# Optimization experiments

Hardware: AMD Instinct MI355X
Metric: run time of the kernel (lower is better)

Reference implementation:

```python
import jax, jax.numpy as jnp
import numpy as np
from jax import lax

MAXIMIZE = True  # matches init_kwargs

def setup_inputs() -> dict:
    key = jax.random.key(0)
    cost_matrix = jax.random.normal(key, (1024, 16384), dtype=jnp.float32)
    return {"cost_matrix": cost_matrix}

def _greedy_assign(cost_matrix):
    n_rows, n_cols = cost_matrix.shape
    n_assign = min(n_rows, n_cols)
    # maximize=True -> keep costs as-is; else negate (matches torch module)
    costs = cost_matrix if MAXIMIZE else -cost_matrix
    neg_inf = jnp.array(-jnp.inf, dtype=costs.dtype)

    def step(carry, _):
        row_used, col_used = carry  # bool [n_rows], bool [n_cols]
        mask = row_used[:, None] | col_used[None, :]
        masked = jnp.where(mask, neg_inf, costs)
        flat = jnp.argmax(masked)  # row-major flat argmax, same as torch reshape(-1).argmax()
        r = flat // n_cols
        c = flat % n_cols
        row_used = row_used.at[r].set(True)
        col_used = col_used.at[c].set(True)
        return (row_used, col_used), (r, c)

    init = (jnp.zeros(n_rows, dtype=bool), jnp.zeros(n_cols, dtype=bool))
    _, (rows, cols) = lax.scan(step, init, None, length=n_assign)
    rows = rows.astype(jnp.int64) if rows.dtype != jnp.int64 else rows
    cols = cols.astype(jnp.int64) if cols.dtype != jnp.int64 else cols
    sort_idx = jnp.argsort(rows)
    return rows[sort_idx], cols[sort_idx]

def reference(cost_matrix):
    row_ind, col_ind = _greedy_assign(cost_matrix)
    return (row_ind, col_ind)
```

## Files before the change

kernel.cpp:

```cpp
#include <hip/hip_runtime.h>
#include <stdint.h>

#define NROWS 1024
#define NCOLS 16384
#define NROUNDS 3

typedef unsigned long long u64;
typedef unsigned int u32;

__device__ u64 g_rowbest[NROWS];
__device__ u64 g_colbest[NCOLS];
__device__ int g_col_used[NCOLS];
__device__ int g_row_assigned[NROWS];
__device__ int g_col_of_row[NROWS];
__device__ int g_remaining[NROWS];
__device__ int g_nrem;

__device__ __forceinline__ u32 fsort(float x) {
    u32 u = __float_as_uint(x);
    return u ^ ((u32)((int)u >> 31) | 0x80000000u);
}

__global__ void k_init(int* __restrict__ out) {
    int i = blockIdx.x * blockDim.x + threadIdx.x;
    if (i < NCOLS) { g_colbest[i] = 0ULL; g_col_used[i] = 0; }
    if (i < NROWS) {
        g_rowbest[i] = 0ULL; g_col_of_row[i] = 0; g_row_assigned[i] = 0;
        out[i] = i;
    }
    if (i == 0) g_nrem = 0;
}

__global__ void k_rowmax(const float* __restrict__ cost) {
    int r = blockIdx.x;
    const float4* row = (const float4*)(cost + (size_t)r * NCOLS);
    u64 best = 0ULL;
    for (int k = threadIdx.x; k < NCOLS / 4; k += blockDim.x) {
        float4 v = row[k];
        int c0 = k * 4;
        u64 k0 = ((u64)fsort(v.x) << 32) | (u32)(NCOLS - 1 - (c0 + 0));
        u64 k1 = ((u64)fsort(v.y) << 32) | (u32)(NCOLS - 1 - (c0 + 1));
        u64 k2 = ((u64)fsort(v.z) << 32) | (u32)(NCOLS - 1 - (c0 + 2));
        u64 k3 = ((u64)fsort(v.w) << 32) | (u32)(NCOLS - 1 - (c0 + 3));
        if (k0 > best) best = k0;
        if (k1 > best) best = k1;
        if (k2 > best) best = k2;
        if (k3 > best) best = k3;
    }
    for (int off = 32; off; off >>= 1) {
        u64 o = __shfl_down(best, off);
        if (o > best) best = o;
    }
    __shared__ u64 part[4];
    int wave = threadIdx.x >> 6;
    if ((threadIdx.x & 63) == 0) part[wave] = best;
    __syncthreads();
    if (threadIdx.x == 0) {
        u64 b = part[0];
        for (int w = 1; w < 4; w++) if (part[w] > b) b = part[w];
        g_rowbest[r] = b;
    }
}

__global__ void k_colmax(const float* __restrict__ cost) {
    int c0 = blockIdx.x * 1024 + threadIdx.x * 4;
    int r0 = blockIdx.y * 64;
    u64 b0 = 0, b1 = 0, b2 = 0, b3 = 0;
    for (int r = r0; r < r0 + 64; ++r) {
        float4 v = *(const float4*)(cost + (size_t)r * NCOLS + c0);
        u32 rk = (u32)(NROWS - 1 - r);
        u64 k0 = ((u64)fsort(v.x) << 32) | rk;
        u64 k1 = ((u64)fsort(v.y) << 32) | rk;
        u64 k2 = ((u64)fsort(v.z) << 32) | rk;
        u64 k3 = ((u64)fsort(v.w) << 32) | rk;
        if (k0 > b0) b0 = k0;
        if (k1 > b1) b1 = k1;
        if (k2 > b2) b2 = k2;
        if (k3 > b3) b3 = k3;
    }
    atomicMax(&g_colbest[c0 + 0], b0);
    atomicMax(&g_colbest[c0 + 1], b1);
    atomicMax(&g_colbest[c0 + 2], b2);
    atomicMax(&g_colbest[c0 + 3], b3);
}

__global__ void k_commit1(int* __restrict__ out) {
    int r = threadIdx.x;
    u64 key = g_rowbest[r];
    int c = NCOLS - 1 - (int)(key & 0xFFFFFFFFu);
    u64 mykey_at_c = (key & 0xFFFFFFFF00000000ULL) | (u32)(NROWS - 1 - r);
    if (g_colbest[c] == mykey_at_c) {
        g_col_used[c] = 1;
        g_col_of_row[r] = c;
        g_row_assigned[r] = 1;
        out[NROWS + r] = c;
    } else {
        int p = atomicAdd(&g_nrem, 1);
        g_remaining[p] = r;
    }
}

__global__ void k_recompute(const float* __restrict__ cost) {
    int r = blockIdx.x;
    if (g_row_assigned[r]) return;
    u64 key = g_rowbest[r];
    int cbest = NCOLS - 1 - (int)(key & 0xFFFFFFFFu);
    if (!g_col_used[cbest]) return;

    u64 best = 0ULL;
    const float4* row = (const float4*)(cost + (size_t)r * NCOLS);
    const int4* used = (const int4*)g_col_used;
    for (int k = threadIdx.x; k < NCOLS / 4; k += blockDim.x) {
        float4 v = row[k];
        int4 u = used[k];
        int c0 = k * 4;
        if (!u.x) { u64 kk = ((u64)fsort(v.x) << 32) | (u32)(NCOLS - 1 - (c0 + 0)); if (kk > best) best = kk; }
        if (!u.y) { u64 kk = ((u64)fsort(v.y) << 32) | (u32)(NCOLS - 1 - (c0 + 1)); if (kk > best) best = kk; }
        if (!u.z) { u64 kk = ((u64)fsort(v.z) << 32) | (u32)(NCOLS - 1 - (c0 + 2)); if (kk > best) best = kk; }
        if (!u.w) { u64 kk = ((u64)fsort(v.w) << 32) | (u32)(NCOLS - 1 - (c0 + 3)); if (kk > best) best = kk; }
    }
    for (int off = 32; off; off >>= 1) {
        u64 o = __shfl_down(best, off);
        if (o > best) best = o;
    }
    __shared__ u64 part[4];
    int wave = threadIdx.x >> 6;
    if ((threadIdx.x & 63) == 0) part[wave] = best;
    __syncthreads();
    if (threadIdx.x == 0) {
        u64 b = part[0];
        for (int w = 1; w < 4; w++) if (part[w] > b) b = part[w];
        g_rowbest[r] = b;
    }
}

__global__ void k_round(const float* __restrict__ cost, int* __restrict__ out) {
    __shared__ int s_list[NROWS];
    __shared__ int s_cand[NROWS];
    __shared__ u64 s_mine[NROWS];
    __shared__ u64 s_max[NROWS];
    __shared__ int s_n;
    int tid = threadIdx.x;
    if (tid == 0) s_n = 0;
    __syncthreads();
    int r = tid;
    bool unassigned = !g_row_assigned[r];
    int mypos = -1;
    if (unassigned) { mypos = atomicAdd(&s_n, 1); s_list[mypos] = r; }
    __syncthreads();
    int n = s_n;
    if (n == 0) { if (tid == 0) g_nrem = 0; return; }

    if (unassigned) {
        u64 key = g_rowbest[r];
        int c = NCOLS - 1 - (int)(key & 0xFFFFFFFFu);
        s_cand[mypos] = c;
        s_mine[mypos] = (key & 0xFFFFFFFF00000000ULL) | (u32)(NROWS - 1 - r);
        s_max[mypos] = 0ULL;
    }
    __syncthreads();

    for (int idx = tid; idx < n * n; idx += blockDim.x) {
        int i = idx / n;
        int j = idx - i * n;
        int c = s_cand[i];
        int rj = s_list[j];
        float x = cost[(size_t)rj * NCOLS + c];
        u64 kj = ((u64)fsort(x) << 32) | (u32)(NROWS - 1 - rj);
        atomicMax(&s_max[i], kj);
    }
    __syncthreads();

    bool win = unassigned && (s_max[mypos] == s_mine[mypos]);
    if (win) {
        int c = s_cand[mypos];
        g_col_used[c] = 1;
        g_col_of_row[r] = c;
        g_row_assigned[r] = 1;
        out[NROWS + r] = c;
    }
    __syncthreads();
    if (tid == 0) s_n = 0;
    __syncthreads();
    if (unassigned && !win) {
        int p = atomicAdd(&s_n, 1);
        g_remaining[p] = r;
    }
    __syncthreads();
    if (tid == 0) g_nrem = s_n;
}

__global__ void k_finish(const float* __restrict__ cost, int* __restrict__ out) {
    __shared__ int s_rem[2][NROWS];
    __shared__ int s_n, s_newn;
    __shared__ u64 s_part[16];
    int tid = threadIdx.x;
    if (tid == 0) s_n = g_nrem;
    __syncthreads();
    int n = s_n;
    if (n == 0) return;
    for (int i = tid; i < n; i += blockDim.x) s_rem[0][i] = g_remaining[i];
    __syncthreads();
    int cur = 0;

    while (n > 0) {
        for (int i = 0; i < n; i++) {
            int r = s_rem[cur][i];
            u64 key = g_rowbest[r];
            int c = NCOLS - 1 - (int)(key & 0xFFFFFFFFu);
            if (g_col_used[c]) {
                u64 best = 0ULL;
                const float4* row = (const float4*)(cost + (size_t)r * NCOLS);
                for (int k = tid; k < NCOLS / 4; k += blockDim.x) {
                    float4 v = row[k];
                    int c0 = k * 4;
                    if (!g_col_used[c0 + 0]) { u64 kk = ((u64)fsort(v.x) << 32) | (u32)(NCOLS - 1 - (c0 + 0)); if (kk > best) best = kk; }
                    if (!g_col_used[c0 + 1]) { u64 kk = ((u64)fsort(v.y) << 32) | (u32)(NCOLS - 1 - (c0 + 1)); if (kk > best) best = kk; }
                    if (!g_col_used[c0 + 2]) { u64 kk = ((u64)fsort(v.z) << 32) | (u32)(NCOLS - 1 - (c0 + 2)); if (kk > best) best = kk; }
                    if (!g_col_used[c0 + 3]) { u64 kk = ((u64)fsort(v.w) << 32) | (u32)(NCOLS - 1 - (c0 + 3)); if (kk > best) best = kk; }
                }
                for (int off = 32; off; off >>= 1) {
                    u64 o = __shfl_down(best, off);
                    if (o > best) best = o;
                }
                int wave = tid >> 6;
                if ((tid & 63) == 0) s_part[wave] = best;
                __syncthreads();
                if (tid == 0) {
                    u64 b = s_part[0];
                    for (int w = 1; w < 16; w++) if (s_part[w] > b) b = s_part[w];
                    g_rowbest[r] = b;
                }
                __syncthreads();
            }
        }
        __syncthreads();

        bool win = false; int myr = -1, myc = -1;
        if (tid < n) {
            int r = s_rem[cur][tid];
            u64 key = g_rowbest[r];
            int c = NCOLS - 1 - (int)(key & 0xFFFFFFFFu);
            u64 mine = (key & 0xFFFFFFFF00000000ULL) | (u32)(NROWS - 1 - r);
            win = true;
            for (int j = 0; j < n; j++) {
                int rj = s_rem[cur][j];
                if (rj == r) continue;
                float x = cost[(size_t)rj * NCOLS + c];
                u64 kj = ((u64)fsort(x) << 32) | (u32)(NROWS - 1 - rj);
                if (kj > mine) { win = false; break; }
            }
            myr = r; myc = c;
        }
        __syncthreads();
        if (win) {
            g_col_used[myc] = 1;
            g_col_of_row[myr] = myc;
            g_row_assigned[myr] = 1;
            out[NROWS + myr] = myc;
        }
        if (tid == 0) s_newn = 0;
        __syncthreads();
        if (tid < n && !win) {
            int p = atomicAdd(&s_newn, 1);
            s_rem[cur ^ 1][p] = myr;
        }
        __syncthreads();
        n = s_newn;
        cur ^= 1;
        __syncthreads();
    }
}

extern "C" void kernel_launch(void* const* d_in, const int* in_sizes, int n_in,
                              void* d_out, int out_size, void* d_ws, size_t ws_size,
                              hipStream_t stream) {
    const float* cost = (const float*)d_in[0];
    int* out = (int*)d_out;

    k_init<<<NCOLS / 256, 256, 0, stream>>>(out);
    k_rowmax<<<NROWS, 256, 0, stream>>>(cost);
    k_colmax<<<dim3(NCOLS / 1024, NROWS / 64), 256, 0, stream>>>(cost);
    k_commit1<<<1, 1024, 0, stream>>>(out);
    for (int round = 0; round < NROUNDS; ++round) {
        k_recompute<<<NROWS, 256, 0, stream>>>(cost);
        k_round<<<1, 1024, 0, stream>>>(cost, out);
    }
    k_finish<<<1, 1024, 0, stream>>>(cost, out);
}
```

Measured before the change: 156.4 us.

## Fuse greedy assignment into one persistent cooperative kernel with grid syncs

Replaces the chain of small launches (init, rowmax, colmax, commit, three recompute/round pairs, single-block finish) with one cooperative kernel of 256 blocks. Each block owns four rows and iterates rounds of masked row-max recompute plus a conflict check, separated by grid.sync, until no rows remain. This removes per-launch overhead and the serial single-block finish loop, which processed remaining rows one at a time. In exchange it adds grid-wide barriers per round, and the per-row conflict check now scans all remaining rows per block. A multi-kernel fallback runs if the cooperative launch fails.

```diff
diff --git a/kernel.cpp b/kernel.cpp
--- a/kernel.cpp
+++ b/kernel.cpp
@@ -1,37 +1,192 @@
 #include <hip/hip_runtime.h>
+#include <hip/hip_cooperative_groups.h>
 #include <stdint.h>
 
 #define NROWS 1024
 #define NCOLS 16384
-#define NROUNDS 3
+#define NBLK  256
+#define NTHR  256
+#define MAXR  1026
 
 typedef unsigned long long u64;
 typedef unsigned int u32;
+
+namespace cg = cooperative_groups;
 
 __device__ u64 g_rowbest[NROWS];
 __device__ u64 g_colbest[NCOLS];
 __device__ int g_col_used[NCOLS];
 __device__ int g_row_assigned[NROWS];
-__device__ int g_col_of_row[NROWS];
-__device__ int g_remaining[NROWS];
-__device__ int g_nrem;
+__device__ int g_rem[2][NROWS];
+__device__ int g_cnt[MAXR];
+__device__ int g_nrem_fb;
 
 __device__ __forceinline__ u32 fsort(float x) {
     u32 u = __float_as_uint(x);
     return u ^ ((u32)((int)u >> 31) | 0x80000000u);
 }
 
-__global__ void k_init(int* __restrict__ out) {
+__device__ __forceinline__ u64 block_reduce_max(u64 v, u64* s_part) {
+    for (int off = 32; off; off >>= 1) {
+        u64 o = __shfl_down(v, off);
+        if (o > v) v = o;
+    }
+    int wave = threadIdx.x >> 6;
+    if ((threadIdx.x & 63) == 0) s_part[wave] = v;
+    __syncthreads();
+    u64 b = s_part[0];
+    for (int w = 1; w < NTHR / 64; w++) if (s_part[w] > b) b = s_part[w];
+    __syncthreads();
+    return b;
+}
+
+__global__ void __launch_bounds__(NTHR) k_lsa(const float* __restrict__ cost,
+                                              int* __restrict__ out) {
+    cg::grid_group grid = cg::this_grid();
+    __shared__ u64 s_part[NTHR / 64];
+    const int tid = threadIdx.x;
+    const int b = blockIdx.x;
+    const int gtid = b * NTHR + tid;
+
+    for (int i = gtid; i < NCOLS; i += NBLK * NTHR) { g_colbest[i] = 0ULL; g_col_used[i] = 0; }
+    if (gtid < NROWS) { g_row_assigned[gtid] = 0; out[gtid] = gtid; }
+    if (gtid < MAXR) g_cnt[gtid] = 0;
+
+    for (int ri = 0; ri < 4; ri++) {
+        int r = b * 4 + ri;
+        const float4* row = (const float4*)(cost + (size_t)r * NCOLS);
+        u64 best = 0ULL;
+        for (int k = tid; k < NCOLS / 4; k += NTHR) {
+            float4 v = row[k];
+            int c0 = k * 4;
+            u64 k0 = ((u64)fsort(v.x) << 32) | (u32)(NCOLS - 1 - (c0 + 0));
+            u64 k1 = ((u64)fsort(v.y) << 32) | (u32)(NCOLS - 1 - (c0 + 1));
+            u64 k2 = ((u64)fsort(v.z) << 32) | (u32)(NCOLS - 1 - (c0 + 2));
+            u64 k3 = ((u64)fsort(v.w) << 32) | (u32)(NCOLS - 1 - (c0 + 3));
+            if (k0 > best) best = k0;
+            if (k1 > best) best = k1;
+            if (k2 > best) best = k2;
+            if (k3 > best) best = k3;
+        }
+        u64 bb = block_reduce_max(best, s_part);
+        if (tid == 0) g_rowbest[r] = bb;
+    }
+    __threadfence();
+    grid.sync();
+
+    {
+        int c0 = (b & 15) * 1024 + tid * 4;
+        int r0 = (b >> 4) * 64;
+        u64 b0 = 0, b1 = 0, b2 = 0, b3 = 0;
+        for (int r = r0; r < r0 + 64; ++r) {
+            float4 v = *(const float4*)(cost + (size_t)r * NCOLS + c0);
+            u32 rk = (u32)(NROWS - 1 - r);
+            u64 k0 = ((u64)fsort(v.x) << 32) | rk;
+            u64 k1 = ((u64)fsort(v.y) << 32) | rk;
+            u64 k2 = ((u64)fsort(v.z) << 32) | rk;
+            u64 k3 = ((u64)fsort(v.w) << 32) | rk;
+            if (k0 > b0) b0 = k0;
+            if (k1 > b1) b1 = k1;
+            if (k2 > b2) b2 = k2;
+            if (k3 > b3) b3 = k3;
+        }
+        atomicMax(&g_colbest[c0 + 0], b0);
+        atomicMax(&g_colbest[c0 + 1], b1);
+        atomicMax(&g_colbest[c0 + 2], b2);
+        atomicMax(&g_colbest[c0 + 3], b3);
+    }
+    __threadfence();
+    grid.sync();
+
+    if (tid < 4) {
+        int r = b * 4 + tid;
+        u64 key = g_rowbest[r];
+        int c = NCOLS - 1 - (int)(key & 0xFFFFFFFFu);
+        u64 mk = (key & 0xFFFFFFFF00000000ULL) | (u32)(NROWS - 1 - r);
+        if (g_colbest[c] == mk) {
+            g_col_used[c] = 1;
+            g_row_assigned[r] = 1;
+            out[NROWS + r] = c;
+        } else {
+            int p = atomicAdd(&g_cnt[0], 1);
+            g_rem[0][p] = r;
+        }
+    }
+    __threadfence();
+    grid.sync();
+
+    int t = 0;
+    while (t < MAXR - 1) {
+        int n = g_cnt[t];
+        if (n == 0) break;
+        const int* list = g_rem[t & 1];
+
+        for (int ri = 0; ri < 4; ri++) {
+            int r = b * 4 + ri;
+            if (g_row_assigned[r]) continue;
+            u64 key = g_rowbest[r];
+            int cb = NCOLS - 1 - (int)(key & 0xFFFFFFFFu);
+            if (!g_col_used[cb]) continue;
+            u64 best = 0ULL;
+            const float4* row = (const float4*)(cost + (size_t)r * NCOLS);
+            const int4* used = (const int4*)g_col_used;
+            for (int k = tid; k < NCOLS / 4; k += NTHR) {
+                float4 v = row[k];
+                int4 u = used[k];
+                int c0 = k * 4;
+                if (!u.x) { u64 kk = ((u64)fsort(v.x) << 32) | (u32)(NCOLS - 1 - (c0 + 0)); if (kk > best) best = kk; }
+                if (!u.y) { u64 kk = ((u64)fsort(v.y) << 32) | (u32)(NCOLS - 1 - (c0 + 1)); if (kk > best) best = kk; }
+                if (!u.z) { u64 kk = ((u64)fsort(v.z) << 32) | (u32)(NCOLS - 1 - (c0 + 2)); if (kk > best) best = kk; }
+                if (!u.w) { u64 kk = ((u64)fsort(v.w) << 32) | (u32)(NCOLS - 1 - (c0 + 3)); if (kk > best) best = kk; }
+            }
+            u64 bb = block_reduce_max(best, s_part);
+            if (tid == 0) g_rowbest[r] = bb;
+            __syncthreads();
+        }
+
+        for (int ri = 0; ri < 4; ri++) {
+            int r = b * 4 + ri;
+            if (g_row_assigned[r]) continue;
+            u64 key = g_rowbest[r];
+            int c = NCOLS - 1 - (int)(key & 0xFFFFFFFFu);
+            u64 mine = (key & 0xFFFFFFFF00000000ULL) | (u32)(NROWS - 1 - r);
+            u64 mx = 0ULL;
+            for (int j = tid; j < n; j += NTHR) {
+                int rj = list[j];
+                if (rj != r) {
+                    float x = cost[(size_t)rj * NCOLS + c];
+                    u64 kj = ((u64)fsort(x) << 32) | (u32)(NROWS - 1 - rj);
+                    if (kj > mx) mx = kj;
+                }
+            }
+            mx = block_reduce_max(mx, s_part);
+            if (tid == 0) {
+                if (mine > mx) {
+                    g_col_used[c] = 1;
+                    g_row_assigned[r] = 1;
+                    out[NROWS + r] = c;
+                } else {
+                    int p = atomicAdd(&g_cnt[t + 1], 1);
+                    g_rem[(t + 1) & 1][p] = r;
+                }
+            }
+            __syncthreads();
+        }
+        __threadfence();
+        grid.sync();
+        t++;
+    }
+}
+
+__global__ void k_init_fb(int* __restrict__ out) {
     int i = blockIdx.x * blockDim.x + threadIdx.x;
     if (i < NCOLS) { g_colbest[i] = 0ULL; g_col_used[i] = 0; }
-    if (i < NROWS) {
-        g_rowbest[i] = 0ULL; g_col_of_row[i] = 0; g_row_assigned[i] = 0;
-        out[i] = i;
-    }
-    if (i == 0) g_nrem = 0;
-}
-
-__global__ void k_rowmax(const float* __restrict__ cost) {
+    if (i < NROWS) { g_row_assigned[i] = 0; out[i] = i; }
+    if (i < MAXR) g_cnt[i] = 0;
+    if (i == 0) g_nrem_fb = 0;
+}
+
+__global__ void k_rowmax_fb(const float* __restrict__ cost) {
     int r = blockIdx.x;
     const float4* row = (const float4*)(cost + (size_t)r * NCOLS);
     u64 best = 0ULL;
@@ -47,22 +202,12 @@
         if (k2 > best) best = k2;
         if (k3 > best) best = k3;
     }
-    for (int off = 32; off; off >>= 1) {
-        u64 o = __shfl_down(best, off);
-        if (o > best) best = o;
-    }
-    __shared__ u64 part[4];
-    int wave = threadIdx.x >> 6;
-    if ((threadIdx.x & 63) == 0) part[wave] = best;
-    __syncthreads();
-    if (threadIdx.x == 0) {
-        u64 b = part[0];
-        for (int w = 1; w < 4; w++) if (part[w] > b) b = part[w];
-        g_rowbest[r] = b;
-    }
-}
-
-__global__ void k_colmax(const float* __restrict__ cost) {
+    __shared__ u64 s_part[NTHR / 64];
+    u64 bb = block_reduce_max(best, s_part);
+    if (threadIdx.x == 0) g_rowbest[r] = bb;
+}
+
+__global__ void k_colmax_fb(const float* __restrict__ cost) {
     int c0 = blockIdx.x * 1024 + threadIdx.x * 4;
     int r0 = blockIdx.y * 64;
     u64 b0 = 0, b1 = 0, b2 = 0, b3 = 0;
@@ -84,125 +229,31 @@
     atomicMax(&g_colbest[c0 + 3], b3);
 }
 
-__global__ void k_commit1(int* __restrict__ out) {
+__global__ void k_commit1_fb(int* __restrict__ out) {
     int r = threadIdx.x;
     u64 key = g_rowbest[r];
     int c = NCOLS - 1 - (int)(key & 0xFFFFFFFFu);
-    u64 mykey_at_c = (key & 0xFFFFFFFF00000000ULL) | (u32)(NROWS - 1 - r);
-    if (g_colbest[c] == mykey_at_c) {
-        g_col_used[c] = 1;
-        g_col_of_row[r] = c;
-        g_row_assigned[r] = 1;
-        out[NROWS + r] = c;
+    u64 mk = (key & 0xFFFFFFFF00000000ULL) | (u32)(NROWS - 1 - r);
+    if (g_colbest[c] == mk) {
+        g_col_used[c] = 1; g_row_assigned[r] = 1; out[NROWS + r] = c;
     } else {
-        int p = atomicAdd(&g_nrem, 1);
-        g_remaining[p] = r;
-    }
-}
-
-__global__ void k_recompute(const float* __restrict__ cost) {
-    int r = blockIdx.x;
-    if (g_row_assigned[r]) return;
-    u64 key = g_rowbest[r];
-    int cbest = NCOLS - 1 - (int)(key & 0xFFFFFFFFu);
-    if (!g_col_used[cbest]) return;
-
-    u64 best = 0ULL;
-    const float4* row = (const float4*)(cost + (size_t)r * NCOLS);
-    const int4* used = (const int4*)g_col_used;
-    for (int k = threadIdx.x; k < NCOLS / 4; k += blockDim.x) {
-        float4 v = row[k];
-        int4 u = used[k];
-        int c0 = k * 4;
-        if (!u.x) { u64 kk = ((u64)fsort(v.x) << 32) | (u32)(NCOLS - 1 - (c0 + 0)); if (kk > best) best = kk; }
-        if (!u.y) { u64 kk = ((u64)fsort(v.y) << 32) | (u32)(NCOLS - 1 - (c0 + 1)); if (kk > best) best = kk; }
-        if (!u.z) { u64 kk = ((u64)fsort(v.z) << 32) | (u32)(NCOLS - 1 - (c0 + 2)); if (kk > best) best = kk; }
-        if (!u.w) { u64 kk = ((u64)fsort(v.w) << 32) | (u32)(NCOLS - 1 - (c0 + 3)); if (kk > best) best = kk; }
-    }
-    for (int off = 32; off; off >>= 1) {
-        u64 o = __shfl_down(best, off);
-        if (o > best) best = o;
-    }
-    __shared__ u64 part[4];
-    int wave = threadIdx.x >> 6;
-    if ((threadIdx.x & 63) == 0) part[wave] = best;
-    __syncthreads();
-    if (threadIdx.x == 0) {
-        u64 b = part[0];
-        for (int w = 1; w < 4; w++) if (part[w] > b) b = part[w];
-        g_rowbest[r] = b;
-    }
-}
-
-__global__ void k_round(const float* __restrict__ cost, int* __restrict__ out) {
-    __shared__ int s_list[NROWS];
-    __shared__ int s_cand[NROWS];
-    __shared__ u64 s_mine[NROWS];
-    __shared__ u64 s_max[NROWS];
-    __shared__ int s_n;
-    int tid = threadIdx.x;
-    if (tid == 0) s_n = 0;
-    __syncthreads();
-    int r = tid;
-    bool unassigned = !g_row_assigned[r];
-    int mypos = -1;
-    if (unassigned) { mypos = atomicAdd(&s_n, 1); s_list[mypos] = r; }
-    __syncthreads();
-    int n = s_n;
-    if (n == 0) { if (tid == 0) g_nrem = 0; return; }
-
-    if (unassigned) {
-        u64 key = g_rowbest[r];
-        int c = NCOLS - 1 - (int)(key & 0xFFFFFFFFu);
-        s_cand[mypos] = c;
-        s_mine[mypos] = (key & 0xFFFFFFFF00000000ULL) | (u32)(NROWS - 1 - r);
-        s_max[mypos] = 0ULL;
-    }
-    __syncthreads();
-
-    for (int idx = tid; idx < n * n; idx += blockDim.x) {
-        int i = idx / n;
-        int j = idx - i * n;
-        int c = s_cand[i];
-        int rj = s_list[j];
-        float x = cost[(size_t)rj * NCOLS + c];
-        u64 kj = ((u64)fsort(x) << 32) | (u32)(NROWS - 1 - rj);
-        atomicMax(&s_max[i], kj);
-    }
-    __syncthreads();
-
-    bool win = unassigned && (s_max[mypos] == s_mine[mypos]);
-    if (win) {
-        int c = s_cand[mypos];
-        g_col_used[c] = 1;
-        g_col_of_row[r] = c;
-        g_row_assigned[r] = 1;
-        out[NROWS + r] = c;
-    }
-    __syncthreads();
-    if (tid == 0) s_n = 0;
-    __syncthreads();
-    if (unassigned && !win) {
-        int p = atomicAdd(&s_n, 1);
-        g_remaining[p] = r;
-    }
-    __syncthreads();
-    if (tid == 0) g_nrem = s_n;
-}
-
-__global__ void k_finish(const float* __restrict__ cost, int* __restrict__ out) {
+        int p = atomicAdd(&g_nrem_fb, 1);
+        g_rem[0][p] = r;
+    }
+}
+
+__global__ void k_finish_fb(const float* __restrict__ cost, int* __restrict__ out) {
     __shared__ int s_rem[2][NROWS];
     __shared__ int s_n, s_newn;
-    __shared__ u64 s_part[16];
+    __shared__ u64 s_part2[16];
     int tid = threadIdx.x;
-    if (tid == 0) s_n = g_nrem;
+    if (tid == 0) s_n = g_nrem_fb;
     __syncthreads();
     int n = s_n;
     if (n == 0) return;
-    for (int i = tid; i < n; i += blockDim.x) s_rem[0][i] = g_remaining[i];
+    for (int i = tid; i < n; i += blockDim.x) s_rem[0][i] = g_rem[0][i];
     __syncthreads();
     int cur = 0;
-
     while (n > 0) {
         for (int i = 0; i < n; i++) {
             int r = s_rem[cur][i];
@@ -224,18 +275,17 @@
                     if (o > best) best = o;
                 }
                 int wave = tid >> 6;
-                if ((tid & 63) == 0) s_part[wave] = best;
+                if ((tid & 63) == 0) s_part2[wave] = best;
                 __syncthreads();
                 if (tid == 0) {
-                    u64 b = s_part[0];
-                    for (int w = 1; w < 16; w++) if (s_part[w] > b) b = s_part[w];
+                    u64 b = s_part2[0];
+                    for (int w = 1; w < 16; w++) if (s_part2[w] > b) b = s_part2[w];
                     g_rowbest[r] = b;
                 }
                 __syncthreads();
             }
         }
         __syncthreads();
-
         bool win = false; int myr = -1, myc = -1;
         if (tid < n) {
             int r = s_rem[cur][tid];
@@ -254,10 +304,7 @@
         }
         __syncthreads();
         if (win) {
-            g_col_used[myc] = 1;
-            g_col_of_row[myr] = myc;
-            g_row_assigned[myr] = 1;
-            out[NROWS + myr] = myc;
+            g_col_used[myc] = 1; g_row_assigned[myr] = 1; out[NROWS + myr] = myc;
         }
         if (tid == 0) s_newn = 0;
         __syncthreads();
@@ -278,13 +325,15 @@
     const float* cost = (const float*)d_in[0];
     int* out = (int*)d_out;
 
-    k_init<<<NCOLS / 256, 256, 0, stream>>>(out);
-    k_rowmax<<<NROWS, 256, 0, stream>>>(cost);
-    k_colmax<<<dim3(NCOLS / 1024, NROWS / 64), 256, 0, stream>>>(cost);
-    k_commit1<<<1, 1024, 0, stream>>>(out);
-    for (int round = 0; round < NROUNDS; ++round) {
-        k_recompute<<<NROWS, 256, 0, stream>>>(cost);
-        k_round<<<1, 1024, 0, stream>>>(cost, out);
-    }
-    k_finish<<<1, 1024, 0, stream>>>(cost, out);
-}
+    void* args[] = { (void*)&cost, (void*)&out };
+    hipError_t err = hipLaunchCooperativeKernel((const void*)k_lsa,
+                                                dim3(NBLK), dim3(NTHR),
+                                                args, 0, stream);
+    if (err != hipSuccess) {
+        k_init_fb<<<NCOLS / 256, 256, 0, stream>>>(out);
+        k_rowmax_fb<<<NROWS, NTHR, 0, stream>>>(cost);
+        k_colmax_fb<<<dim3(NCOLS / 1024, NROWS / 64), 256, 0, stream>>>(cost);
+        k_commit1_fb<<<1, 1024, 0, stream>>>(out);
+        k_finish_fb<<<1, 1024, 0, stream>>>(cost, out);
+    }
+}
```

Result: slower. 408.2 us (+160.9%).
